# Kernel optimization log

Measured on AMD Instinct MI355X. Metric: run time of the kernel, lower is better.

## Reference

```python
import jax, jax.numpy as jnp
import numpy as np

B, S, D, H, F, E = 4, 1024, 1024, 16, 4096, 8
HD = D // H  # head dim


def setup_inputs() -> dict:
    key = jax.random.key(0)
    ks = jax.random.split(key, 8)
    p = lambda k, shp: jax.random.normal(k, shp, jnp.float32) * 0.02
    return {
        "x": jax.random.normal(ks[0], (B, S, D), jnp.float32),
        "mask": jnp.ones((B, S), jnp.int32),
        "in_proj_w": p(ks[1], (3 * D, D)),
        "in_proj_b": jnp.zeros((3 * D,), jnp.float32),
        "out_proj_w": p(ks[2], (D, D)),
        "out_proj_b": jnp.zeros((D,), jnp.float32),
        "ln1_g": jnp.ones((D,), jnp.float32),
        "ln1_b": jnp.zeros((D,), jnp.float32),
        "ln2_g": jnp.ones((D,), jnp.float32),
        "ln2_b": jnp.zeros((D,), jnp.float32),
        "gate_w": p(ks[3], (E, D)),
        "gate_b": jnp.zeros((E,), jnp.float32),
        "w1": p(ks[4], (E, F, D)),
        "b1": jnp.zeros((E, F), jnp.float32),
        "w2": p(ks[5], (E, D, F)),
        "b2": jnp.zeros((E, D), jnp.float32),
    }


def _layernorm(x, g, b, eps=1e-5):
    m = x.mean(-1, keepdims=True)
    v = ((x - m) ** 2).mean(-1, keepdims=True)
    return (x - m) / jnp.sqrt(v + eps) * g + b


def _mha(x, key_pad, in_proj_w, in_proj_b, out_proj_w, out_proj_b):
    # combined QKV projection as in torch nn.MultiheadAttention
    qkv = x @ in_proj_w.T + in_proj_b  # (B,S,3D)
    q, k, v = jnp.split(qkv, 3, axis=-1)
    def heads(t):
        return t.reshape(B, S, H, HD).transpose(0, 2, 1, 3)  # (B,H,S,HD)
    q, k, v = heads(q), heads(k), heads(v)
    scores = jnp.einsum("bhqd,bhkd->bhqk", q, k) / jnp.sqrt(jnp.float32(HD))
    scores = jnp.where(key_pad[:, None, None, :], -1e30, scores)
    attn = jax.nn.softmax(scores, axis=-1)
    out = jnp.einsum("bhqk,bhkd->bhqd", attn, v)  # (B,H,S,HD)
    out = out.transpose(0, 2, 1, 3).reshape(B, S, D)
    return out @ out_proj_w.T + out_proj_b


def _moe(x, gate_w, gate_b, w1, b1, w2, b2):
    logits = x @ gate_w.T + gate_b            # (B,S,E)
    probs = jax.nn.softmax(logits, axis=-1)
    # dense all-expert FFN (faithful to original: every expert computed)
    h = jax.nn.relu(jnp.einsum("bsd,efd->bsef", x, w1) + b1)   # (B,S,E,F)
    all_out = jnp.einsum("bsef,edf->bsed", h, w2) + b2          # (B,S,E,D)
    top_vals, top_idx = jax.lax.top_k(probs, 2)                 # (B,S,2)
    weights = top_vals / (top_vals.sum(-1, keepdims=True) + 1e-9)
    sel = jnp.take_along_axis(all_out, top_idx[..., None], axis=2)  # (B,S,2,D)
    return (sel * weights[..., None]).sum(axis=2)


def reference(x, mask, in_proj_w, in_proj_b, out_proj_w, out_proj_b,
              ln1_g, ln1_b, ln2_g, ln2_b, gate_w, gate_b, w1, b1, w2, b2):
    key_pad = mask == 0  # (B,S) bool
    attn_out = _mha(x, key_pad, in_proj_w, in_proj_b, out_proj_w, out_proj_b)
    x1 = _layernorm(x + attn_out, ln1_g, ln1_b)
    ff = _moe(x1, gate_w, gate_b, w1, b1, w2, b2)
    return _layernorm(x1 + ff, ln2_g, ln2_b)
```

## Files before the change

### kernel.cpp

```cpp
#include <hip/hip_runtime.h>

typedef __attribute__((ext_vector_type(8))) short bf16x8;
typedef __attribute__((ext_vector_type(4))) float f32x4;

#define DEV __device__ __forceinline__

static constexpr int Bb = 4, Sq = 1024, Dd = 1024, Hh = 16, HDd = 64, Ff = 4096, Ee = 8;
static constexpr int Nn = Bb * Sq;
static constexpr int TD = 3 * Dd;
static constexpr int PMAX = 2 * Nn + Ee * 128;

DEV unsigned short f2bf(float x) {
  union { float f; unsigned u; } c; c.f = x;
  unsigned r = c.u + 0x7FFFu + ((c.u >> 16) & 1u);
  return (unsigned short)(r >> 16);
}

typedef const __attribute__((address_space(1))) unsigned int* gas_t;
typedef __attribute__((address_space(3))) unsigned int* las_t;
DEV void gload16(const void* g, void* l) {
  __builtin_amdgcn_global_load_lds((gas_t)g, (las_t)l, 16, 0, 0);
}

__global__ __launch_bounds__(256) void cvt_kernel(const float* __restrict__ in,
                                                  unsigned short* __restrict__ out) {
  int i = blockIdx.x * 256 + threadIdx.x;
  const float4 a = *(const float4*)(in + (size_t)i * 8);
  const float4 b = *(const float4*)(in + (size_t)i * 8 + 4);
  union { uint4 u; unsigned short s[8]; } pk;
  pk.s[0] = f2bf(a.x); pk.s[1] = f2bf(a.y); pk.s[2] = f2bf(a.z); pk.s[3] = f2bf(a.w);
  pk.s[4] = f2bf(b.x); pk.s[5] = f2bf(b.y); pk.s[6] = f2bf(b.z); pk.s[7] = f2bf(b.w);
  *(uint4*)(out + (size_t)i * 8) = pk.u;
}

template <int EPI>
__global__ __launch_bounds__(256) void gemm_bt(
    const unsigned short* __restrict__ A, const unsigned short* __restrict__ Bw,
    const float* __restrict__ bias, void* __restrict__ o0, void* __restrict__ o1,
    void* __restrict__ o2, int M, int Ncols, int K,
    const int* __restrict__ poff) {
  int bx, by;
  {
    const int gx = gridDim.x, nwg = gx * gridDim.y;
    int orig = blockIdx.y * gx + blockIdx.x;
    int q = nwg >> 3, r = nwg & 7;
    int xcd = orig & 7, lin = orig >> 3;
    int wg = (xcd < r ? xcd * (q + 1) : r * (q + 1) + (xcd - r) * q) + lin;
    bx = wg % gx; by = wg / gx;
  }
  const int m0 = bx * 128;
  int e = 0;
  if constexpr (EPI >= 2) {
    if (m0 >= poff[Ee]) return;
#pragma unroll
    for (int k = 1; k < Ee; ++k) if (m0 >= poff[k]) e = k;
  } else {
    if (m0 >= M) return;
  }
  const int n0 = by * 128;
  const unsigned short* Bptr = Bw + (size_t)e * Ncols * K;
  const float* biasptr = bias + e * Ncols;

  __shared__ __align__(128) unsigned short As[3 * 128 * 32];
  __shared__ __align__(128) unsigned short Bs[3 * 128 * 32];

  const int tid = threadIdx.x;
  const int lane = tid & 63, wid = tid >> 6;
  const int wm = wid >> 1, wn = wid & 1;
  const int lr = lane & 15, lk = lane >> 4;

  const char* aSrc[2]; const char* bSrc[2];
  int dOff[2];
#pragma unroll
  for (int it = 0; it < 2; ++it) {
    int b = it * 4096 + tid * 16;
    int r = b >> 6;
    int colb = (b & 63) ^ (((r >> 1) & 3) << 4);
    aSrc[it] = (const char*)(A + (size_t)(m0 + r) * K) + colb;
    bSrc[it] = (const char*)(Bptr + (size_t)(n0 + r) * K) + colb;
    dOff[it] = it * 4096 + wid * 1024;
  }
  int aOff[4], bOff[4];
#pragma unroll
  for (int i = 0; i < 4; ++i) {
    int ra = wm * 64 + i * 16 + lr;
    aOff[i] = ra * 32 + ((lk ^ ((ra >> 1) & 3)) << 3);
    int rb = wn * 64 + i * 16 + lr;
    bOff[i] = rb * 32 + ((lk ^ ((rb >> 1) & 3)) << 3);
  }

  auto STAGE = [&](int t, int buf) {
#pragma unroll
    for (int it = 0; it < 2; ++it) {
      gload16(aSrc[it] + (size_t)t * 64, (char*)As + buf * 8192 + dOff[it]);
      gload16(bSrc[it] + (size_t)t * 64, (char*)Bs + buf * 8192 + dOff[it]);
    }
  };

  f32x4 acc[4][4] = {};
  const int NT = K >> 5;

  STAGE(0, 0);
  STAGE(1, 1);
  int cb = 0;
  int sb = 2;
  for (int t = 0; t < NT; ++t) {
    if (t + 1 < NT) asm volatile("s_waitcnt vmcnt(4)" ::: "memory");
    else            asm volatile("s_waitcnt vmcnt(0)" ::: "memory");
    __builtin_amdgcn_sched_barrier(0);
    __builtin_amdgcn_s_barrier();
    __builtin_amdgcn_sched_barrier(0);
    if (t + 2 < NT) STAGE(t + 2, sb);
    const unsigned short* Ab = As + cb * 4096;
    const unsigned short* Bb2 = Bs + cb * 4096;
    bf16x8 af[4], bfv[4];
#pragma unroll
    for (int mi = 0; mi < 4; ++mi) af[mi] = *(const bf16x8*)&Ab[aOff[mi]];
#pragma unroll
    for (int ni = 0; ni < 4; ++ni) bfv[ni] = *(const bf16x8*)&Bb2[bOff[ni]];
#pragma unroll
    for (int mi = 0; mi < 4; ++mi)
#pragma unroll
      for (int ni = 0; ni < 4; ++ni)
        acc[mi][ni] = __builtin_amdgcn_mfma_f32_16x16x32_bf16(af[mi], bfv[ni], acc[mi][ni], 0, 0, 0);
    cb = (cb == 2) ? 0 : cb + 1;
    sb = (sb == 2) ? 0 : sb + 1;
  }

#pragma unroll
  for (int ni = 0; ni < 4; ++ni) {
    const int col = n0 + wn * 64 + ni * 16 + lr;
    const float bv = biasptr[col];
#pragma unroll
    for (int mi = 0; mi < 4; ++mi) {
#pragma unroll
      for (int i = 0; i < 4; ++i) {
        const int mloc = wm * 64 + mi * 16 + lk * 4 + i;
        float v = acc[mi][ni][i] + bv;
        if constexpr (EPI == 0) {
          int t = m0 + mloc;
          int which = col >> 10, jj = col & 1023, hh = jj >> 6, hd = jj & 63;
          int bb = t >> 10, s = t & 1023;
          unsigned short* dst = (which == 0) ? (unsigned short*)o0
                              : (which == 1) ? (unsigned short*)o1 : (unsigned short*)o2;
          dst[((size_t)(bb * Hh + hh) * Sq + s) * HDd + hd] = f2bf(v);
        } else if constexpr (EPI == 1) {
          ((float*)o0)[(size_t)(m0 + mloc) * Dd + col] = v;
        } else if constexpr (EPI == 2) {
          ((unsigned short*)o0)[(size_t)(m0 + mloc) * Ff + col] = f2bf(fmaxf(v, 0.f));
        } else {
          ((float*)o0)[(size_t)(m0 + mloc) * Dd + col] = v;
        }
      }
    }
  }
}

__global__ __launch_bounds__(256) void attn_kernel(
    const unsigned short* __restrict__ qb, const unsigned short* __restrict__ kb,
    const unsigned short* __restrict__ vb, const int* __restrict__ mask,
    unsigned short* __restrict__ attnb) {
  const int qt = blockIdx.x, h = blockIdx.y, b = blockIdx.z;
  const unsigned short* Q = qb + (size_t)(b * Hh + h) * Sq * HDd;
  const unsigned short* Kg = kb + (size_t)(b * Hh + h) * Sq * HDd;
  const unsigned short* Vg = vb + (size_t)(b * Hh + h) * Sq * HDd;

  __shared__ unsigned short Qs[64 * 72], Ks[64 * 72], Vt[64 * 72], Ps[64 * 72];
  __shared__ float Ssm[64 * 65];
  __shared__ float mS[64], lS[64], aS[64];
  __shared__ int mk[64];

  const int tid = threadIdx.x, lane = tid & 63, wid = tid >> 6;
  const int lr = lane & 15, lk = lane >> 4;

#pragma unroll
  for (int it = 0; it < 2; ++it) {
    int c = tid + it * 256; int r = c >> 3, kc = (c & 7) * 8;
    *(uint4*)&Qs[r * 72 + kc] = *(const uint4*)(Q + (size_t)(qt * 64 + r) * 64 + kc);
  }
  if (tid < 64) { mS[tid] = -1e30f; lS[tid] = 0.f; }

  f32x4 oacc[4] = {};

  for (int kt = 0; kt < 16; ++kt) {
    __syncthreads();
#pragma unroll
    for (int it = 0; it < 2; ++it) {
      int c = tid + it * 256; int r = c >> 3, kc = (c & 7) * 8;
      *(uint4*)&Ks[r * 72 + kc] = *(const uint4*)(Kg + (size_t)(kt * 64 + r) * 64 + kc);
    }
    {
      int kk = tid >> 2, hg = (tid & 3) * 16;
      union { uint4 u[2]; unsigned short s[16]; } tv;
      tv.u[0] = *(const uint4*)(Vg + (size_t)(kt * 64 + kk) * 64 + hg);
      tv.u[1] = *(const uint4*)(Vg + (size_t)(kt * 64 + kk) * 64 + hg + 8);
#pragma unroll
      for (int j = 0; j < 16; ++j) Vt[(hg + j) * 72 + kk] = tv.s[j];
    }
    if (tid < 64) mk[tid] = mask[b * Sq + kt * 64 + tid];
    __syncthreads();

    f32x4 sacc[4] = {};
#pragma unroll
    for (int ks = 0; ks < 2; ++ks) {
      bf16x8 aq = *(const bf16x8*)&Qs[(wid * 16 + lr) * 72 + ks * 32 + lk * 8];
#pragma unroll
      for (int ni = 0; ni < 4; ++ni) {
        bf16x8 bk = *(const bf16x8*)&Ks[(ni * 16 + lr) * 72 + ks * 32 + lk * 8];
        sacc[ni] = __builtin_amdgcn_mfma_f32_16x16x32_bf16(aq, bk, sacc[ni], 0, 0, 0);
      }
    }
#pragma unroll
    for (int ni = 0; ni < 4; ++ni)
#pragma unroll
      for (int i = 0; i < 4; ++i) {
        int r = wid * 16 + lk * 4 + i, cc = ni * 16 + lr;
        float v = sacc[ni][i] * 0.125f;
        if (mk[cc] == 0) v = -1e30f;
        Ssm[r * 65 + cc] = v;
      }
    __syncthreads();
    {
      int r = tid >> 2, cg = (tid & 3) * 16;
      float xv[16];
#pragma unroll
      for (int j = 0; j < 16; ++j) xv[j] = Ssm[r * 65 + cg + j];
      float mx = xv[0];
#pragma unroll
      for (int j = 1; j < 16; ++j) mx = fmaxf(mx, xv[j]);
      mx = fmaxf(mx, __shfl_xor(mx, 1));
      mx = fmaxf(mx, __shfl_xor(mx, 2));
      float mprev = mS[r];
      float mnew = fmaxf(mprev, mx);
      float sum = 0.f;
      union { uint4 u[2]; unsigned short s[16]; } pb;
#pragma unroll
      for (int j = 0; j < 16; ++j) {
        float pv = expf(xv[j] - mnew);
        sum += pv; pb.s[j] = f2bf(pv);
      }
      sum += __shfl_xor(sum, 1);
      sum += __shfl_xor(sum, 2);
      *(uint4*)&Ps[r * 72 + cg] = pb.u[0];
      *(uint4*)&Ps[r * 72 + cg + 8] = pb.u[1];
      if ((tid & 3) == 0) {
        float alpha = expf(mprev - mnew);
        mS[r] = mnew; aS[r] = alpha; lS[r] = lS[r] * alpha + sum;
      }
    }
    __syncthreads();
#pragma unroll
    for (int ni = 0; ni < 4; ++ni)
#pragma unroll
      for (int i = 0; i < 4; ++i)
        oacc[ni][i] *= aS[wid * 16 + lk * 4 + i];
#pragma unroll
    for (int ks = 0; ks < 2; ++ks) {
      bf16x8 ap = *(const bf16x8*)&Ps[(wid * 16 + lr) * 72 + ks * 32 + lk * 8];
#pragma unroll
      for (int ni = 0; ni < 4; ++ni) {
        bf16x8 bv = *(const bf16x8*)&Vt[(ni * 16 + lr) * 72 + ks * 32 + lk * 8];
        oacc[ni] = __builtin_amdgcn_mfma_f32_16x16x32_bf16(ap, bv, oacc[ni], 0, 0, 0);
      }
    }
  }
  __syncthreads();
#pragma unroll
  for (int ni = 0; ni < 4; ++ni)
#pragma unroll
    for (int i = 0; i < 4; ++i) {
      int r = wid * 16 + lk * 4 + i;
      int q = qt * 64 + r;
      float v = oacc[ni][i] / lS[r];
      attnb[((size_t)(b * Sq + q)) * Dd + h * 64 + ni * 16 + lr] = f2bf(v);
    }
}

__global__ __launch_bounds__(256) void ln_kernel(
    const float* __restrict__ a, const float* __restrict__ b2,
    const float* __restrict__ g, const float* __restrict__ beta,
    float* __restrict__ outf, unsigned short* __restrict__ outb) {
  const int t = blockIdx.x, tid = threadIdx.x;
  float4 v = *(const float4*)(a + (size_t)t * Dd + tid * 4);
  {
    float4 u = *(const float4*)(b2 + (size_t)t * Dd + tid * 4);
    v.x += u.x; v.y += u.y; v.z += u.z; v.w += u.w;
  }
  const int lane = tid & 63, wid = tid >> 6;
  float s = v.x + v.y + v.z + v.w;
  for (int sh = 1; sh < 64; sh <<= 1) s += __shfl_xor(s, sh);
  __shared__ float red[4], red2[4];
  if (lane == 0) red[wid] = s;
  __syncthreads();
  float mean = (red[0] + red[1] + red[2] + red[3]) * (1.f / Dd);
  float dx = v.x - mean, dy = v.y - mean, dz = v.z - mean, dw = v.w - mean;
  float q = dx * dx + dy * dy + dz * dz + dw * dw;
  for (int sh = 1; sh < 64; sh <<= 1) q += __shfl_xor(q, sh);
  if (lane == 0) red2[wid] = q;
  __syncthreads();
  float var = (red2[0] + red2[1] + red2[2] + red2[3]) * (1.f / Dd);
  float rstd = rsqrtf(var + 1e-5f);
  float4 gg = *(const float4*)(g + tid * 4);
  float4 bb = *(const float4*)(beta + tid * 4);
  float4 o;
  o.x = dx * rstd * gg.x + bb.x;
  o.y = dy * rstd * gg.y + bb.y;
  o.z = dz * rstd * gg.z + bb.z;
  o.w = dw * rstd * gg.w + bb.w;
  if (outf) *(float4*)(outf + (size_t)t * Dd + tid * 4) = o;
  if (outb) {
    ushort4 pk; pk.x = f2bf(o.x); pk.y = f2bf(o.y); pk.z = f2bf(o.z); pk.w = f2bf(o.w);
    *(ushort4*)(outb + (size_t)t * Dd + tid * 4) = pk;
  }
}

__global__ __launch_bounds__(256) void ln2_kernel(
    const float* __restrict__ x1f, const float* __restrict__ ffp,
    const int* __restrict__ inv, const float* __restrict__ wtok,
    const float* __restrict__ g, const float* __restrict__ beta,
    float* __restrict__ out) {
  const int t = blockIdx.x, tid = threadIdx.x;
  const int i0 = inv[2 * t], i1 = inv[2 * t + 1];
  const float w0 = wtok[2 * t], w1 = wtok[2 * t + 1];
  float4 v = *(const float4*)(x1f + (size_t)t * Dd + tid * 4);
  float4 u0 = *(const float4*)(ffp + (size_t)i0 * Dd + tid * 4);
  float4 u1 = *(const float4*)(ffp + (size_t)i1 * Dd + tid * 4);
  v.x += w0 * u0.x + w1 * u1.x; v.y += w0 * u0.y + w1 * u1.y;
  v.z += w0 * u0.z + w1 * u1.z; v.w += w0 * u0.w + w1 * u1.w;
  const int lane = tid & 63, wid = tid >> 6;
  float s = v.x + v.y + v.z + v.w;
  for (int sh = 1; sh < 64; sh <<= 1) s += __shfl_xor(s, sh);
  __shared__ float red[4], red2[4];
  if (lane == 0) red[wid] = s;
  __syncthreads();
  float mean = (red[0] + red[1] + red[2] + red[3]) * (1.f / Dd);
  float dx = v.x - mean, dy = v.y - mean, dz = v.z - mean, dw = v.w - mean;
  float q = dx * dx + dy * dy + dz * dz + dw * dw;
  for (int sh = 1; sh < 64; sh <<= 1) q += __shfl_xor(q, sh);
  if (lane == 0) red2[wid] = q;
  __syncthreads();
  float var = (red2[0] + red2[1] + red2[2] + red2[3]) * (1.f / Dd);
  float rstd = rsqrtf(var + 1e-5f);
  float4 gg = *(const float4*)(g + tid * 4);
  float4 bb = *(const float4*)(beta + tid * 4);
  float4 o;
  o.x = dx * rstd * gg.x + bb.x;
  o.y = dy * rstd * gg.y + bb.y;
  o.z = dz * rstd * gg.z + bb.z;
  o.w = dw * rstd * gg.w + bb.w;
  *(float4*)(out + (size_t)t * Dd + tid * 4) = o;
}

__global__ __launch_bounds__(256) void route_kernel(
    const float* __restrict__ x1f, const float* __restrict__ gw, const float* __restrict__ gb,
    int* __restrict__ cnt, int* __restrict__ tokslot, float* __restrict__ wtok) {
  __shared__ float gws[Ee * Dd];
  const int tid = threadIdx.x;
#pragma unroll
  for (int it = 0; it < 8; ++it) {
    int idx = (tid + it * 256) * 4;
    *(float4*)&gws[idx] = *(const float4*)(gw + idx);
  }
  __syncthreads();
  const int lane = tid & 63, wid = tid >> 6;
  for (int it = 0; it < 16; ++it) {
    int t = blockIdx.x * 64 + wid * 16 + it;
    float acc[Ee] = {};
    for (int i = 0; i < 16; ++i) {
      float xv = x1f[(size_t)t * Dd + i * 64 + lane];
#pragma unroll
      for (int e = 0; e < Ee; ++e) acc[e] += xv * gws[e * Dd + i * 64 + lane];
    }
#pragma unroll
    for (int e = 0; e < Ee; ++e) {
      float vv = acc[e];
      for (int sh = 1; sh < 64; sh <<= 1) vv += __shfl_xor(vv, sh);
      acc[e] = vv;
    }
    if (lane == 0) {
      float lg[Ee];
#pragma unroll
      for (int e = 0; e < Ee; ++e) lg[e] = acc[e] + gb[e];
      float m = lg[0];
#pragma unroll
      for (int e = 1; e < Ee; ++e) m = fmaxf(m, lg[e]);
      float p[Ee], ssum = 0.f;
#pragma unroll
      for (int e = 0; e < Ee; ++e) { p[e] = expf(lg[e] - m); ssum += p[e]; }
      int e0 = 0;
#pragma unroll
      for (int e = 1; e < Ee; ++e) if (p[e] > p[e0]) e0 = e;
      int e1 = -1;
#pragma unroll
      for (int e = 0; e < Ee; ++e) {
        if (e == e0) continue;
        if (e1 < 0 || p[e] > p[e1]) e1 = e;
      }
      float v0 = p[e0] / ssum, v1 = p[e1] / ssum;
      float wsum = v0 + v1 + 1e-9f;
      wtok[t * 2] = v0 / wsum; wtok[t * 2 + 1] = v1 / wsum;
      int p0 = atomicAdd(&cnt[e0], 1);
      tokslot[e0 * Nn + p0] = t * 2;
      int p1 = atomicAdd(&cnt[e1], 1);
      tokslot[e1 * Nn + p1] = t * 2 + 1;
    }
  }
}

__global__ void offsets_kernel(const int* __restrict__ cnt, int* __restrict__ poff) {
  if (threadIdx.x == 0) {
    int s = 0;
    for (int e = 0; e < Ee; ++e) { poff[e] = s; s += (cnt[e] + 127) & ~127; }
    poff[Ee] = s;
  }
}

__global__ __launch_bounds__(256) void pack_kernel(
    const unsigned short* __restrict__ x1b, const int* __restrict__ tokslot,
    const int* __restrict__ cnt, const int* __restrict__ poff,
    unsigned short* __restrict__ xg, int* __restrict__ inv) {
  const int tid = threadIdx.x;
  const int g = blockIdx.x * 8 + (tid >> 5);
  const int l = tid & 31;
  if (g >= poff[Ee]) return;
  int e = 0;
#pragma unroll
  for (int k = 1; k < Ee; ++k) if (g >= poff[k]) e = k;
  const int pos = g - poff[e];
  uint4* dst = (uint4*)(xg + (size_t)g * Dd);
  if (pos < cnt[e]) {
    const int ent = tokslot[e * Nn + pos];
    if (l == 0) inv[ent] = g;
    const uint4* src = (const uint4*)(x1b + (size_t)(ent >> 1) * Dd);
#pragma unroll
    for (int j = 0; j < 4; ++j) dst[l + j * 32] = src[l + j * 32];
  } else {
    const uint4 z = make_uint4(0, 0, 0, 0);
#pragma unroll
    for (int j = 0; j < 4; ++j) dst[l + j * 32] = z;
  }
}

extern "C" void kernel_launch(void* const* d_in, const int* in_sizes, int n_in,
                              void* d_out, int out_size, void* d_ws, size_t ws_size,
                              hipStream_t stream) {
  const float* x   = (const float*)d_in[0];
  const int*   msk = (const int*)d_in[1];
  const float* ipw = (const float*)d_in[2];
  const float* ipb = (const float*)d_in[3];
  const float* opw = (const float*)d_in[4];
  const float* opb = (const float*)d_in[5];
  const float* g1  = (const float*)d_in[6];
  const float* be1 = (const float*)d_in[7];
  const float* g2  = (const float*)d_in[8];
  const float* be2 = (const float*)d_in[9];
  const float* gw  = (const float*)d_in[10];
  const float* gb  = (const float*)d_in[11];
  const float* w1  = (const float*)d_in[12];
  const float* b1  = (const float*)d_in[13];
  const float* w2  = (const float*)d_in[14];
  const float* b2  = (const float*)d_in[15];
  float* out = (float*)d_out;

  char* p = (char*)d_ws;
  auto carve = [&](size_t bytes) { char* r = p; p += (bytes + 255) & ~(size_t)255; return r; };
  unsigned short* xb   = (unsigned short*)carve((size_t)Nn * Dd * 2);
  unsigned short* qb   = (unsigned short*)carve((size_t)Nn * Dd * 2);
  unsigned short* kb   = (unsigned short*)carve((size_t)Nn * Dd * 2);
  unsigned short* vb   = (unsigned short*)carve((size_t)Nn * Dd * 2);
  float* proj          = (float*)carve((size_t)Nn * Dd * 4);
  float* x1f           = (float*)carve((size_t)Nn * Dd * 4);
  unsigned short* x1b  = (unsigned short*)carve((size_t)Nn * Dd * 2);
  unsigned short* xg   = (unsigned short*)carve((size_t)PMAX * Dd * 2);
  float* ffp           = (float*)carve((size_t)PMAX * Dd * 4);
  unsigned short* hbuf = (unsigned short*)carve((size_t)PMAX * Ff * 2);
  unsigned short* wbuf = (unsigned short*)carve((size_t)Ee * Ff * Dd * 2);
  int* cnt             = (int*)carve(64);
  int* poff            = (int*)carve(64);
  int* tokslot         = (int*)carve((size_t)Ee * Nn * 4);
  float* wtok          = (float*)carve((size_t)2 * Nn * 4);
  int* inv             = (int*)carve((size_t)2 * Nn * 4);
  unsigned short* attnb = xb;

  cvt_kernel<<<Nn * Dd / 2048, 256, 0, stream>>>(x, xb);
  cvt_kernel<<<TD * Dd / 2048, 256, 0, stream>>>(ipw, wbuf);
  gemm_bt<0><<<dim3(Nn / 128, TD / 128), 256, 0, stream>>>(
      xb, wbuf, ipb, qb, kb, vb, Nn, TD, Dd, nullptr);
  attn_kernel<<<dim3(Sq / 64, Hh, Bb), 256, 0, stream>>>(qb, kb, vb, msk, attnb);
  cvt_kernel<<<Dd * Dd / 2048, 256, 0, stream>>>(opw, wbuf);
  gemm_bt<1><<<dim3(Nn / 128, Dd / 128), 256, 0, stream>>>(
      attnb, wbuf, opb, proj, nullptr, nullptr, Nn, Dd, Dd, nullptr);
  ln_kernel<<<Nn, 256, 0, stream>>>(x, proj, g1, be1, x1f, x1b);
  hipMemsetAsync(cnt, 0, 64, stream);
  route_kernel<<<Nn / 64, 256, 0, stream>>>(x1f, gw, gb, cnt, tokslot, wtok);
  offsets_kernel<<<1, 64, 0, stream>>>(cnt, poff);
  pack_kernel<<<PMAX / 8, 256, 0, stream>>>(x1b, tokslot, cnt, poff, xg, inv);
  cvt_kernel<<<Ee * Ff * Dd / 2048, 256, 0, stream>>>(w1, wbuf);
  gemm_bt<2><<<dim3(PMAX / 128, Ff / 128), 256, 0, stream>>>(
      xg, wbuf, b1, hbuf, nullptr, nullptr, PMAX, Ff, Dd, poff);
  cvt_kernel<<<Ee * Dd * Ff / 2048, 256, 0, stream>>>(w2, wbuf);
  gemm_bt<3><<<dim3(PMAX / 128, Dd / 128), 256, 0, stream>>>(
      hbuf, wbuf, b2, ffp, nullptr, nullptr, PMAX, Dd, Ff, poff);
  ln2_kernel<<<Nn, 256, 0, stream>>>(x1f, ffp, inv, wtok, g2, be2, out);
}
```

Before: 627.5 us.

## Fuse fp32 weight conversion into GEMMs, add split-K, fuse LN1 with routing

Removes the separate fp32-to-bf16 conversion passes over every weight matrix. The GEMM now reads fp32 B tiles straight from global memory into registers and packs them to bf16 in-loop with v_cvt_pk_bf16_f32, so only A goes through LDS. The out-projection and second expert GEMM use a 2-way split-K that writes two partial buffers; the following layernorm kernels sum them. The gating/top-2 routing is folded into the LN1 kernel, and expert group padding grows to 256 rows. The cost is that B is no longer shared through LDS, so each wave re-reads fp32 weights from global memory and needs more registers, plus extra partial-sum traffic.

```diff
diff --git a/kernel.cpp b/kernel.cpp
--- a/kernel.cpp
+++ b/kernel.cpp
@@ -8,7 +8,7 @@
 static constexpr int Bb = 4, Sq = 1024, Dd = 1024, Hh = 16, HDd = 64, Ff = 4096, Ee = 8;
 static constexpr int Nn = Bb * Sq;
 static constexpr int TD = 3 * Dd;
-static constexpr int PMAX = 2 * Nn + Ee * 128;
+static constexpr int PMAX = 2 * Nn + Ee * 256;
 
 DEV unsigned short f2bf(float x) {
   union { float f; unsigned u; } c; c.f = x;
@@ -20,6 +20,15 @@
 typedef __attribute__((address_space(3))) unsigned int* las_t;
 DEV void gload16(const void* g, void* l) {
   __builtin_amdgcn_global_load_lds((gas_t)g, (las_t)l, 16, 0, 0);
+}
+
+DEV bf16x8 cvt8(float4 a, float4 b) {
+  union { unsigned u[4]; bf16x8 v; } r;
+  asm("v_cvt_pk_bf16_f32 %0, %1, %2" : "=v"(r.u[0]) : "v"(a.x), "v"(a.y));
+  asm("v_cvt_pk_bf16_f32 %0, %1, %2" : "=v"(r.u[1]) : "v"(a.z), "v"(a.w));
+  asm("v_cvt_pk_bf16_f32 %0, %1, %2" : "=v"(r.u[2]) : "v"(b.x), "v"(b.y));
+  asm("v_cvt_pk_bf16_f32 %0, %1, %2" : "=v"(r.u[3]) : "v"(b.z), "v"(b.w));
+  return r.v;
 }
 
 __global__ __launch_bounds__(256) void cvt_kernel(const float* __restrict__ in,
@@ -33,21 +42,24 @@
   *(uint4*)(out + (size_t)i * 8) = pk.u;
 }
 
-template <int EPI>
+DEV void xcd_swz(int& bx, int& by, int gx, int gy) {
+  const int nwg = gx * gy;
+  int orig = by * gx + bx;
+  int q = nwg >> 3, r = nwg & 7;
+  int xcd = orig & 7, lin = orig >> 3;
+  int wg = (xcd < r ? xcd * (q + 1) : r * (q + 1) + (xcd - r) * q) + lin;
+  bx = wg / gy; by = wg % gy;
+}
+
+template <int EPI, int KS = 1>
 __global__ __launch_bounds__(256) void gemm_bt(
-    const unsigned short* __restrict__ A, const unsigned short* __restrict__ Bw,
+    const unsigned short* __restrict__ A, const float* __restrict__ Bw,
     const float* __restrict__ bias, void* __restrict__ o0, void* __restrict__ o1,
     void* __restrict__ o2, int M, int Ncols, int K,
     const int* __restrict__ poff) {
-  int bx, by;
-  {
-    const int gx = gridDim.x, nwg = gx * gridDim.y;
-    int orig = blockIdx.y * gx + blockIdx.x;
-    int q = nwg >> 3, r = nwg & 7;
-    int xcd = orig & 7, lin = orig >> 3;
-    int wg = (xcd < r ? xcd * (q + 1) : r * (q + 1) + (xcd - r) * q) + lin;
-    bx = wg % gx; by = wg / gx;
-  }
+  const int kh = (KS > 1) ? blockIdx.z : 0;
+  int bx = blockIdx.x, by = blockIdx.y;
+  xcd_swz(bx, by, gridDim.x, gridDim.y);
   const int m0 = bx * 128;
   int e = 0;
   if constexpr (EPI >= 2) {
@@ -58,66 +70,79 @@
     if (m0 >= M) return;
   }
   const int n0 = by * 128;
-  const unsigned short* Bptr = Bw + (size_t)e * Ncols * K;
+  const int Kloc = K / KS;
+  const int k00 = kh * Kloc;
+  const float* Bptr = Bw + (size_t)e * Ncols * K;
   const float* biasptr = bias + e * Ncols;
 
   __shared__ __align__(128) unsigned short As[3 * 128 * 32];
-  __shared__ __align__(128) unsigned short Bs[3 * 128 * 32];
 
   const int tid = threadIdx.x;
   const int lane = tid & 63, wid = tid >> 6;
   const int wm = wid >> 1, wn = wid & 1;
   const int lr = lane & 15, lk = lane >> 4;
 
-  const char* aSrc[2]; const char* bSrc[2];
-  int dOff[2];
+  const char* aSrc[2]; int dOff[2];
 #pragma unroll
   for (int it = 0; it < 2; ++it) {
     int b = it * 4096 + tid * 16;
     int r = b >> 6;
     int colb = (b & 63) ^ (((r >> 1) & 3) << 4);
-    aSrc[it] = (const char*)(A + (size_t)(m0 + r) * K) + colb;
-    bSrc[it] = (const char*)(Bptr + (size_t)(n0 + r) * K) + colb;
+    aSrc[it] = (const char*)(A + (size_t)(m0 + r) * K + k00) + colb;
     dOff[it] = it * 4096 + wid * 1024;
   }
-  int aOff[4], bOff[4];
+  int aOff[4];
 #pragma unroll
   for (int i = 0; i < 4; ++i) {
     int ra = wm * 64 + i * 16 + lr;
     aOff[i] = ra * 32 + ((lk ^ ((ra >> 1) & 3)) << 3);
-    int rb = wn * 64 + i * 16 + lr;
-    bOff[i] = rb * 32 + ((lk ^ ((rb >> 1) & 3)) << 3);
-  }
-
-  auto STAGE = [&](int t, int buf) {
-#pragma unroll
-    for (int it = 0; it < 2; ++it) {
+  }
+  const float* bBase[4];
+#pragma unroll
+  for (int ni = 0; ni < 4; ++ni)
+    bBase[ni] = Bptr + (size_t)(n0 + wn * 64 + ni * 16 + lr) * K + k00 + lk * 8;
+
+  auto ST_A = [&](int t, int buf) {
+#pragma unroll
+    for (int it = 0; it < 2; ++it)
       gload16(aSrc[it] + (size_t)t * 64, (char*)As + buf * 8192 + dOff[it]);
-      gload16(bSrc[it] + (size_t)t * 64, (char*)Bs + buf * 8192 + dOff[it]);
-    }
   };
 
   f32x4 acc[4][4] = {};
-  const int NT = K >> 5;
-
-  STAGE(0, 0);
-  STAGE(1, 1);
-  int cb = 0;
-  int sb = 2;
+  float4 br[8];
+  const int NT = Kloc >> 5;
+
+  ST_A(0, 0);
+#pragma unroll
+  for (int ni = 0; ni < 4; ++ni) {
+    br[2 * ni] = *(const float4*)(bBase[ni]);
+    br[2 * ni + 1] = *(const float4*)(bBase[ni] + 4);
+  }
+  ST_A(1, 1);
+
+  int cb = 0, sb = 2;
   for (int t = 0; t < NT; ++t) {
-    if (t + 1 < NT) asm volatile("s_waitcnt vmcnt(4)" ::: "memory");
+    if (t + 1 < NT) asm volatile("s_waitcnt vmcnt(2)" ::: "memory");
     else            asm volatile("s_waitcnt vmcnt(0)" ::: "memory");
+    __builtin_amdgcn_sched_barrier(0);
+    bf16x8 bfv[4];
+#pragma unroll
+    for (int ni = 0; ni < 4; ++ni) bfv[ni] = cvt8(br[2 * ni], br[2 * ni + 1]);
+    if (t + 1 < NT) {
+#pragma unroll
+      for (int ni = 0; ni < 4; ++ni) {
+        br[2 * ni] = *(const float4*)(bBase[ni] + (t + 1) * 32);
+        br[2 * ni + 1] = *(const float4*)(bBase[ni] + (t + 1) * 32 + 4);
+      }
+    }
     __builtin_amdgcn_sched_barrier(0);
     __builtin_amdgcn_s_barrier();
     __builtin_amdgcn_sched_barrier(0);
-    if (t + 2 < NT) STAGE(t + 2, sb);
+    if (t + 2 < NT) ST_A(t + 2, sb);
     const unsigned short* Ab = As + cb * 4096;
-    const unsigned short* Bb2 = Bs + cb * 4096;
-    bf16x8 af[4], bfv[4];
+    bf16x8 af[4];
 #pragma unroll
     for (int mi = 0; mi < 4; ++mi) af[mi] = *(const bf16x8*)&Ab[aOff[mi]];
-#pragma unroll
-    for (int ni = 0; ni < 4; ++ni) bfv[ni] = *(const bf16x8*)&Bb2[bOff[ni]];
 #pragma unroll
     for (int mi = 0; mi < 4; ++mi)
 #pragma unroll
@@ -130,7 +155,7 @@
 #pragma unroll
   for (int ni = 0; ni < 4; ++ni) {
     const int col = n0 + wn * 64 + ni * 16 + lr;
-    const float bv = biasptr[col];
+    const float bv = (kh == 0) ? biasptr[col] : 0.f;
 #pragma unroll
     for (int mi = 0; mi < 4; ++mi) {
 #pragma unroll
@@ -145,11 +170,11 @@
                               : (which == 1) ? (unsigned short*)o1 : (unsigned short*)o2;
           dst[((size_t)(bb * Hh + hh) * Sq + s) * HDd + hd] = f2bf(v);
         } else if constexpr (EPI == 1) {
-          ((float*)o0)[(size_t)(m0 + mloc) * Dd + col] = v;
+          ((float*)o0)[(size_t)(kh * Nn + m0 + mloc) * Dd + col] = v;
         } else if constexpr (EPI == 2) {
           ((unsigned short*)o0)[(size_t)(m0 + mloc) * Ff + col] = f2bf(fmaxf(v, 0.f));
         } else {
-          ((float*)o0)[(size_t)(m0 + mloc) * Dd + col] = v;
+          ((float*)o0)[(size_t)(kh * PMAX + m0 + mloc) * Dd + col] = v;
         }
       }
     }
@@ -276,20 +301,25 @@
     }
 }
 
-__global__ __launch_bounds__(256) void ln_kernel(
-    const float* __restrict__ a, const float* __restrict__ b2,
+__global__ __launch_bounds__(256) void ln1_route_kernel(
+    const float* __restrict__ a, const float* __restrict__ p0,
+    const float* __restrict__ p1,
     const float* __restrict__ g, const float* __restrict__ beta,
-    float* __restrict__ outf, unsigned short* __restrict__ outb) {
+    const float* __restrict__ gw, const float* __restrict__ gb,
+    float* __restrict__ outf, unsigned short* __restrict__ outb,
+    int* __restrict__ cnt, int* __restrict__ tokslot, float* __restrict__ wtok) {
   const int t = blockIdx.x, tid = threadIdx.x;
   float4 v = *(const float4*)(a + (size_t)t * Dd + tid * 4);
   {
-    float4 u = *(const float4*)(b2 + (size_t)t * Dd + tid * 4);
-    v.x += u.x; v.y += u.y; v.z += u.z; v.w += u.w;
+    float4 u = *(const float4*)(p0 + (size_t)t * Dd + tid * 4);
+    float4 u2 = *(const float4*)(p1 + (size_t)t * Dd + tid * 4);
+    v.x += u.x + u2.x; v.y += u.y + u2.y; v.z += u.z + u2.z; v.w += u.w + u2.w;
   }
   const int lane = tid & 63, wid = tid >> 6;
   float s = v.x + v.y + v.z + v.w;
   for (int sh = 1; sh < 64; sh <<= 1) s += __shfl_xor(s, sh);
   __shared__ float red[4], red2[4];
+  __shared__ float gred[4 * Ee];
   if (lane == 0) red[wid] = s;
   __syncthreads();
   float mean = (red[0] + red[1] + red[2] + red[3]) * (1.f / Dd);
@@ -301,16 +331,58 @@
   float var = (red2[0] + red2[1] + red2[2] + red2[3]) * (1.f / Dd);
   float rstd = rsqrtf(var + 1e-5f);
   float4 gg = *(const float4*)(g + tid * 4);
-  float4 bb = *(const float4*)(beta + tid * 4);
+  float4 bbv = *(const float4*)(beta + tid * 4);
   float4 o;
-  o.x = dx * rstd * gg.x + bb.x;
-  o.y = dy * rstd * gg.y + bb.y;
-  o.z = dz * rstd * gg.z + bb.z;
-  o.w = dw * rstd * gg.w + bb.w;
-  if (outf) *(float4*)(outf + (size_t)t * Dd + tid * 4) = o;
-  if (outb) {
+  o.x = dx * rstd * gg.x + bbv.x;
+  o.y = dy * rstd * gg.y + bbv.y;
+  o.z = dz * rstd * gg.z + bbv.z;
+  o.w = dw * rstd * gg.w + bbv.w;
+  *(float4*)(outf + (size_t)t * Dd + tid * 4) = o;
+  {
     ushort4 pk; pk.x = f2bf(o.x); pk.y = f2bf(o.y); pk.z = f2bf(o.z); pk.w = f2bf(o.w);
     *(ushort4*)(outb + (size_t)t * Dd + tid * 4) = pk;
+  }
+  float gacc[Ee];
+#pragma unroll
+  for (int e = 0; e < Ee; ++e) {
+    float4 gv = *(const float4*)(gw + (size_t)e * Dd + tid * 4);
+    gacc[e] = o.x * gv.x + o.y * gv.y + o.z * gv.z + o.w * gv.w;
+  }
+#pragma unroll
+  for (int e = 0; e < Ee; ++e)
+    for (int sh = 1; sh < 64; sh <<= 1) gacc[e] += __shfl_xor(gacc[e], sh);
+  if (lane == 0) {
+#pragma unroll
+    for (int e = 0; e < Ee; ++e) gred[wid * Ee + e] = gacc[e];
+  }
+  __syncthreads();
+  if (tid == 0) {
+    float lg[Ee];
+#pragma unroll
+    for (int e = 0; e < Ee; ++e)
+      lg[e] = gred[e] + gred[Ee + e] + gred[2 * Ee + e] + gred[3 * Ee + e] + gb[e];
+    float m = lg[0];
+#pragma unroll
+    for (int e = 1; e < Ee; ++e) m = fmaxf(m, lg[e]);
+    float p[Ee], ssum = 0.f;
+#pragma unroll
+    for (int e = 0; e < Ee; ++e) { p[e] = expf(lg[e] - m); ssum += p[e]; }
+    int e0 = 0;
+#pragma unroll
+    for (int e = 1; e < Ee; ++e) if (p[e] > p[e0]) e0 = e;
+    int e1 = -1;
+#pragma unroll
+    for (int e = 0; e < Ee; ++e) {
+      if (e == e0) continue;
+      if (e1 < 0 || p[e] > p[e1]) e1 = e;
+    }
+    float v0 = p[e0] / ssum, v1 = p[e1] / ssum;
+    float wsum = v0 + v1 + 1e-9f;
+    wtok[t * 2] = v0 / wsum; wtok[t * 2 + 1] = v1 / wsum;
+    int pp0 = atomicAdd(&cnt[e0], 1);
+    tokslot[e0 * Nn + pp0] = t * 2;
+    int pp1 = atomicAdd(&cnt[e1], 1);
+    tokslot[e1 * Nn + pp1] = t * 2 + 1;
   }
 }
 
@@ -322,11 +394,16 @@
   const int t = blockIdx.x, tid = threadIdx.x;
   const int i0 = inv[2 * t], i1 = inv[2 * t + 1];
   const float w0 = wtok[2 * t], w1 = wtok[2 * t + 1];
+  const float* ffp1 = ffp + (size_t)PMAX * Dd;
   float4 v = *(const float4*)(x1f + (size_t)t * Dd + tid * 4);
-  float4 u0 = *(const float4*)(ffp + (size_t)i0 * Dd + tid * 4);
-  float4 u1 = *(const float4*)(ffp + (size_t)i1 * Dd + tid * 4);
-  v.x += w0 * u0.x + w1 * u1.x; v.y += w0 * u0.y + w1 * u1.y;
-  v.z += w0 * u0.z + w1 * u1.z; v.w += w0 * u0.w + w1 * u1.w;
+  float4 a0 = *(const float4*)(ffp + (size_t)i0 * Dd + tid * 4);
+  float4 a1 = *(const float4*)(ffp1 + (size_t)i0 * Dd + tid * 4);
+  float4 b0 = *(const float4*)(ffp + (size_t)i1 * Dd + tid * 4);
+  float4 b1 = *(const float4*)(ffp1 + (size_t)i1 * Dd + tid * 4);
+  v.x += w0 * (a0.x + a1.x) + w1 * (b0.x + b1.x);
+  v.y += w0 * (a0.y + a1.y) + w1 * (b0.y + b1.y);
+  v.z += w0 * (a0.z + a1.z) + w1 * (b0.z + b1.z);
+  v.w += w0 * (a0.w + a1.w) + w1 * (b0.w + b1.w);
   const int lane = tid & 63, wid = tid >> 6;
   float s = v.x + v.y + v.z + v.w;
   for (int sh = 1; sh < 64; sh <<= 1) s += __shfl_xor(s, sh);
@@ -351,66 +428,10 @@
   *(float4*)(out + (size_t)t * Dd + tid * 4) = o;
 }
 
-__global__ __launch_bounds__(256) void route_kernel(
-    const float* __restrict__ x1f, const float* __restrict__ gw, const float* __restrict__ gb,
-    int* __restrict__ cnt, int* __restrict__ tokslot, float* __restrict__ wtok) {
-  __shared__ float gws[Ee * Dd];
-  const int tid = threadIdx.x;
-#pragma unroll
-  for (int it = 0; it < 8; ++it) {
-    int idx = (tid + it * 256) * 4;
-    *(float4*)&gws[idx] = *(const float4*)(gw + idx);
-  }
-  __syncthreads();
-  const int lane = tid & 63, wid = tid >> 6;
-  for (int it = 0; it < 16; ++it) {
-    int t = blockIdx.x * 64 + wid * 16 + it;
-    float acc[Ee] = {};
-    for (int i = 0; i < 16; ++i) {
-      float xv = x1f[(size_t)t * Dd + i * 64 + lane];
-#pragma unroll
-      for (int e = 0; e < Ee; ++e) acc[e] += xv * gws[e * Dd + i * 64 + lane];
-    }
-#pragma unroll
-    for (int e = 0; e < Ee; ++e) {
-      float vv = acc[e];
-      for (int sh = 1; sh < 64; sh <<= 1) vv += __shfl_xor(vv, sh);
-      acc[e] = vv;
-    }
-    if (lane == 0) {
-      float lg[Ee];
-#pragma unroll
-      for (int e = 0; e < Ee; ++e) lg[e] = acc[e] + gb[e];
-      float m = lg[0];
-#pragma unroll
-      for (int e = 1; e < Ee; ++e) m = fmaxf(m, lg[e]);
-      float p[Ee], ssum = 0.f;
-#pragma unroll
-      for (int e = 0; e < Ee; ++e) { p[e] = expf(lg[e] - m); ssum += p[e]; }
-      int e0 = 0;
-#pragma unroll
-      for (int e = 1; e < Ee; ++e) if (p[e] > p[e0]) e0 = e;
-      int e1 = -1;
-#pragma unroll
-      for (int e = 0; e < Ee; ++e) {
-        if (e == e0) continue;
-        if (e1 < 0 || p[e] > p[e1]) e1 = e;
-      }
-      float v0 = p[e0] / ssum, v1 = p[e1] / ssum;
-      float wsum = v0 + v1 + 1e-9f;
-      wtok[t * 2] = v0 / wsum; wtok[t * 2 + 1] = v1 / wsum;
-      int p0 = atomicAdd(&cnt[e0], 1);
-      tokslot[e0 * Nn + p0] = t * 2;
-      int p1 = atomicAdd(&cnt[e1], 1);
-      tokslot[e1 * Nn + p1] = t * 2 + 1;
-    }
-  }
-}
-
 __global__ void offsets_kernel(const int* __restrict__ cnt, int* __restrict__ poff) {
   if (threadIdx.x == 0) {
     int s = 0;
-    for (int e = 0; e < Ee; ++e) { poff[e] = s; s += (cnt[e] + 127) & ~127; }
+    for (int e = 0; e < Ee; ++e) { poff[e] = s; s += (cnt[e] + 255) & ~255; }
     poff[Ee] = s;
   }
 }
@@ -468,13 +489,12 @@
   unsigned short* qb   = (unsigned short*)carve((size_t)Nn * Dd * 2);
   unsigned short* kb   = (unsigned short*)carve((size_t)Nn * Dd * 2);
   unsigned short* vb   = (unsigned short*)carve((size_t)Nn * Dd * 2);
-  float* proj          = (float*)carve((size_t)Nn * Dd * 4);
+  float* proj          = (float*)carve((size_t)2 * Nn * Dd * 4);
   float* x1f           = (float*)carve((size_t)Nn * Dd * 4);
   unsigned short* x1b  = (unsigned short*)carve((size_t)Nn * Dd * 2);
   unsigned short* xg   = (unsigned short*)carve((size_t)PMAX * Dd * 2);
-  float* ffp           = (float*)carve((size_t)PMAX * Dd * 4);
+  float* ffp           = (float*)carve((size_t)2 * PMAX * Dd * 4);
   unsigned short* hbuf = (unsigned short*)carve((size_t)PMAX * Ff * 2);
-  unsigned short* wbuf = (unsigned short*)carve((size_t)Ee * Ff * Dd * 2);
   int* cnt             = (int*)carve(64);
   int* poff            = (int*)carve(64);
   int* tokslot         = (int*)carve((size_t)Ee * Nn * 4);
@@ -483,23 +503,19 @@
   unsigned short* attnb = xb;
 
   cvt_kernel<<<Nn * Dd / 2048, 256, 0, stream>>>(x, xb);
-  cvt_kernel<<<TD * Dd / 2048, 256, 0, stream>>>(ipw, wbuf);
-  gemm_bt<0><<<dim3(Nn / 128, TD / 128), 256, 0, stream>>>(
-      xb, wbuf, ipb, qb, kb, vb, Nn, TD, Dd, nullptr);
+  gemm_bt<0, 1><<<dim3(Nn / 128, TD / 128), 256, 0, stream>>>(
+      xb, ipw, ipb, qb, kb, vb, Nn, TD, Dd, nullptr);
   attn_kernel<<<dim3(Sq / 64, Hh, Bb), 256, 0, stream>>>(qb, kb, vb, msk, attnb);
-  cvt_kernel<<<Dd * Dd / 2048, 256, 0, stream>>>(opw, wbuf);
-  gemm_bt<1><<<dim3(Nn / 128, Dd / 128), 256, 0, stream>>>(
-      attnb, wbuf, opb, proj, nullptr, nullptr, Nn, Dd, Dd, nullptr);
-  ln_kernel<<<Nn, 256, 0, stream>>>(x, proj, g1, be1, x1f, x1b);
+  gemm_bt<1, 2><<<dim3(Nn / 128, Dd / 128, 2), 256, 0, stream>>>(
+      attnb, opw, opb, proj, nullptr, nullptr, Nn, Dd, Dd, nullptr);
   hipMemsetAsync(cnt, 0, 64, stream);
-  route_kernel<<<Nn / 64, 256, 0, stream>>>(x1f, gw, gb, cnt, tokslot, wtok);
+  ln1_route_kernel<<<Nn, 256, 0, stream>>>(x, proj, proj + (size_t)Nn * Dd,
+                                           g1, be1, gw, gb, x1f, x1b, cnt, tokslot, wtok);
   offsets_kernel<<<1, 64, 0, stream>>>(cnt, poff);
   pack_kernel<<<PMAX / 8, 256, 0, stream>>>(x1b, tokslot, cnt, poff, xg, inv);
-  cvt_kernel<<<Ee * Ff * Dd / 2048, 256, 0, stream>>>(w1, wbuf);
-  gemm_bt<2><<<dim3(PMAX / 128, Ff / 128), 256, 0, stream>>>(
-      xg, wbuf, b1, hbuf, nullptr, nullptr, PMAX, Ff, Dd, poff);
-  cvt_kernel<<<Ee * Dd * Ff / 2048, 256, 0, stream>>>(w2, wbuf);
-  gemm_bt<3><<<dim3(PMAX / 128, Dd / 128), 256, 0, stream>>>(
-      hbuf, wbuf, b2, ffp, nullptr, nullptr, PMAX, Dd, Ff, poff);
+  gemm_bt<2, 1><<<dim3(PMAX / 128, Ff / 128), 256, 0, stream>>>(
+      xg, w1, b1, hbuf, nullptr, nullptr, PMAX, Ff, Dd, poff);
+  gemm_bt<3, 2><<<dim3(PMAX / 128, Dd / 128, 2), 256, 0, stream>>>(
+      hbuf, w2, b2, ffp, nullptr, nullptr, PMAX, Dd, Ff, poff);
   ln2_kernel<<<Nn, 256, 0, stream>>>(x1f, ffp, inv, wtok, g2, be2, out);
 }
```

Result: slower. 1.036 ms (+65.1%).
